# Kernel optimization log

Hardware: AMD Instinct MI355X
Metric: run time of the kernel (lower is better)

## Reference

```python
import jax, jax.numpy as jnp
import numpy as np

T, B, E, H = 2048, 2, 1024, 16
DH = E // H
SCALE = DH ** -0.5
NEG = jnp.finfo(jnp.float32).min


def setup_inputs() -> dict:
    key = jax.random.key(0)
    ks = jax.random.split(key, 10)
    s = 0.02
    query = jax.random.normal(ks[0], (T, B, E), dtype=jnp.float32)
    key_padding_mask = jax.random.randint(ks[1], (B, T), 0, 2).astype(bool)
    # causal additive mask, broadcastable over (bsz, heads, tgt, src)
    causal = jnp.triu(jnp.ones((T, T), dtype=bool), k=1)
    attn_mask = jnp.where(causal, NEG, 0.0).astype(jnp.float32)[None, None]
    Wq = jax.random.normal(ks[2], (E, E), jnp.float32) * s
    bq = jax.random.normal(ks[3], (E,), jnp.float32) * s
    Wk = jax.random.normal(ks[4], (E, E), jnp.float32) * s
    bk = jax.random.normal(ks[5], (E,), jnp.float32) * s
    Wv = jax.random.normal(ks[6], (E, E), jnp.float32) * s
    bv = jax.random.normal(ks[7], (E,), jnp.float32) * s
    Wo = jax.random.normal(ks[8], (E, E), jnp.float32) * s
    bo = jax.random.normal(ks[9], (E,), jnp.float32) * s
    return {"query": query, "key_padding_mask": key_padding_mask, "attn_mask": attn_mask,
            "Wq": Wq, "bq": bq, "Wk": Wk, "bk": bk, "Wv": Wv, "bv": bv, "Wo": Wo, "bo": bo}


def _heads(x):
    # [T, B, E] -> [B, H, T, DH]
    return x.reshape(T, B, H, DH).transpose(1, 2, 0, 3)


def reference(query, key_padding_mask, attn_mask, Wq, bq, Wk, bk, Wv, bv, Wo, bo):
    # projections (torch Linear: x @ W.T + b); q scaled as in module
    q = _heads((query @ Wq.T + bq) * SCALE)          # [B,H,T,DH]
    k = _heads(query @ Wk.T + bk)                    # [B,H,S,DH] (self-attn: S=T)
    v = _heads(query @ Wv.T + bv)
    scores = jnp.einsum('bhtd,bhsd->bhts', q, k)     # [B,H,T,S]
    scores = scores + attn_mask                      # additive causal mask
    # key_padding_mask True -> masked_fill with dtype min
    scores = jnp.where(key_padding_mask[:, None, None, :], NEG, scores)
    probs = jax.nn.softmax(scores, axis=-1)
    ctx = jnp.einsum('bhts,bhsd->bhtd', probs, v)    # [B,H,T,DH]
    ctx = ctx.transpose(2, 0, 1, 3).reshape(T, B, E) # back to [T,B,E]
    return ctx @ Wo.T + bo
```

## Files before the change

kernel.cpp:

```cpp
#include <hip/hip_runtime.h>
#include <hip/hip_bf16.h>
#include <stdint.h>

typedef unsigned short u16;
typedef uint32_t u32;
typedef unsigned long long u64;
typedef __attribute__((ext_vector_type(8))) short bf16x8;
typedef __attribute__((ext_vector_type(4))) float f32x4;
typedef __attribute__((ext_vector_type(16))) float f32x16;
typedef __attribute__((ext_vector_type(2))) unsigned int u32x2;
typedef __attribute__((ext_vector_type(4))) u32 u32x4;

#define T_SEQ 2048

__device__ __forceinline__ float bf2f(u16 u) {
  union { u32 i; float f; } v; v.i = ((u32)u) << 16; return v.f;
}
__device__ __forceinline__ u16 f2bf(float f) {
  union { float f; u32 i; } v; v.f = f;
  u32 u = v.i;
  return (u16)((u + 0x7fffu + ((u >> 16) & 1u)) >> 16);
}

#if __has_builtin(__builtin_amdgcn_exp2f)
#define EXP2F(x) __builtin_amdgcn_exp2f(x)
#else
#define EXP2F(x) exp2f(x)
#endif

__device__ __forceinline__ u32 permpack(float lo, float hi) {
#if __has_builtin(__builtin_amdgcn_perm)
  return __builtin_amdgcn_perm(__float_as_uint(hi), __float_as_uint(lo), 0x07060302u);
#else
  return (__float_as_uint(hi) & 0xFFFF0000u) | (__float_as_uint(lo) >> 16);
#endif
}

__device__ __forceinline__ void plswap(u32& a, u32& b) {
#if __has_builtin(__builtin_amdgcn_permlane32_swap)
  u32x2 r = __builtin_amdgcn_permlane32_swap(a, b, false, false);
  a = r[0]; b = r[1];
#else
  u32 ra = __shfl_xor(a, 32, 64), rb = __shfl_xor(b, 32, 64);
  const bool hi_ = (threadIdx.x & 32) != 0;
  u32 na = hi_ ? rb : a;
  u32 nb = hi_ ? b : ra;
  a = na; b = nb;
#endif
}
__device__ __forceinline__ float othhalf(float x, bool ishi) {
  u32 a = __float_as_uint(x), b = a;
  plswap(a, b);
  return __uint_as_float(ishi ? a : b);
}

__device__ __forceinline__ void gload_lds16(const void* g, void* l) {
  __builtin_amdgcn_global_load_lds(
      (const __attribute__((address_space(1))) void*)g,
      (__attribute__((address_space(3))) void*)l, 16, 0, 0);
}

__global__ __launch_bounds__(256) void cvt5_kernel(
    const float* __restrict__ qsrc, const float* __restrict__ w0,
    const float* __restrict__ w1, const float* __restrict__ w2,
    const float* __restrict__ w3, const int* __restrict__ kpm,
    u16* __restrict__ qbf, u16* __restrict__ wbf, u64* __restrict__ kpmbits) {
  const int bx = blockIdx.x;
  if (bx == 8192) {
    const int wv = threadIdx.x >> 6, lane = threadIdx.x & 63;
    for (int pair = wv; pair < 64; pair += 4) {
      int v = kpm[pair*64 + lane];
      u64 m = __ballot(v != 0);
      if (lane == 0) kpmbits[pair] = m;
    }
    return;
  }
  const float* src; u16* dst; int i;
  if (bx < 4096) {
    src = qsrc; dst = qbf; i = (bx*256 + threadIdx.x)*4;
  } else {
    int t = bx - 4096;
    int z = t >> 10;
    src = (z == 0) ? w0 : (z == 1) ? w1 : (z == 2) ? w2 : w3;
    dst = wbf + (size_t)z * 1048576;
    i = ((t & 1023)*256 + threadIdx.x)*4;
  }
  const float4 v = *(const float4*)(src + i);
  ushort4 o;
  o.x = f2bf(v.x); o.y = f2bf(v.y); o.z = f2bf(v.z); o.w = f2bf(v.w);
  *(ushort4*)(dst + i) = o;
}

__device__ __forceinline__ void gemm_core_128x128(
    f32x4 acc[2][4], const u16* __restrict__ A, const u16* __restrict__ Bw,
    int bm, int bn, u16* As, u16* Bs)
{
  const int tid = threadIdx.x;
  const int w = tid >> 6, lane = tid & 63, g = lane >> 4, c = lane & 15;
  const int wr = (w & 3) * 32, wc = (w >> 2) * 64;
  for (int k0 = 0; k0 < 1024; k0 += 64) {
    __syncthreads();
    #pragma unroll
    for (int is = 0; is < 2; ++is) {
      int o = (is*8 + w)*1024 + lane*16;
      int row = o >> 7, c16 = (o >> 4) & 7;
      gload_lds16(A + (size_t)(bm*128 + row)*1024 + k0 + (c16 ^ (row & 7))*8,
                  (char*)As + (is*8 + w)*1024);
    }
    #pragma unroll
    for (int is = 0; is < 2; ++is) {
      int o = (is*8 + w)*1024 + lane*16;
      int row = o >> 7, c16 = (o >> 4) & 7;
      gload_lds16(Bw + (size_t)(bn*128 + row)*1024 + k0 + (c16 ^ (row & 7))*8,
                  (char*)Bs + (is*8 + w)*1024);
    }
    __syncthreads();
    bf16x8 af[2][2], bfr[4][2];
    #pragma unroll
    for (int mf = 0; mf < 2; ++mf)
      #pragma unroll
      for (int kc = 0; kc < 2; ++kc) {
        int row = wr + mf*16 + c;
        int colb = kc*64 + g*16;
        af[mf][kc] = *(const bf16x8*)((const char*)As + row*128 + (colb ^ ((row & 7) << 4)));
      }
    #pragma unroll
    for (int nf = 0; nf < 4; ++nf)
      #pragma unroll
      for (int kc = 0; kc < 2; ++kc) {
        int row = wc + nf*16 + c;
        int colb = kc*64 + g*16;
        bfr[nf][kc] = *(const bf16x8*)((const char*)Bs + row*128 + (colb ^ ((row & 7) << 4)));
      }
    #pragma unroll
    for (int mf = 0; mf < 2; ++mf)
      #pragma unroll
      for (int nf = 0; nf < 4; ++nf)
        #pragma unroll
        for (int kc = 0; kc < 2; ++kc)
          acc[mf][nf] = __builtin_amdgcn_mfma_f32_16x16x32_bf16(
              af[mf][kc], bfr[nf][kc], acc[mf][nf], 0, 0, 0);
  }
}

__global__ __launch_bounds__(512, 2) void gemm_qkv(
    const u16* __restrict__ Abf, const u16* __restrict__ Wbf,
    const float* __restrict__ bq, const float* __restrict__ bk,
    const float* __restrict__ bv, u16* __restrict__ qkvh)
{
  __shared__ __align__(16) u16 As[128*64];
  __shared__ __align__(16) u16 Bs[128*64];
  f32x4 acc[2][4];
  #pragma unroll
  for (int mf = 0; mf < 2; ++mf)
    #pragma unroll
    for (int nf = 0; nf < 4; ++nf) acc[mf][nf] = (f32x4){0.f,0.f,0.f,0.f};
  const int bx = blockIdx.x;
  const int bm = (bx & 7) * 4 + (bx >> 3);
  gemm_core_128x128(acc, Abf, Wbf, bm, blockIdx.y, As, Bs);
  const int tid = threadIdx.x, w = tid >> 6, lane = tid & 63, g = lane >> 4, c = lane & 15;
  const int wr = (w & 3) * 32, wc = (w >> 2) * 64;
  #pragma unroll
  for (int mf = 0; mf < 2; ++mf)
    #pragma unroll
    for (int nf = 0; nf < 4; ++nf) {
      int col = blockIdx.y*128 + wc + nf*16 + c;
      int z = col >> 10, colz = col & 1023;
      const float* bias = (z == 0) ? bq : (z == 1) ? bk : bv;
      float bcol = bias[colz];
      float scl = (z == 0) ? 0.18033688011112043f : 1.0f;
      int h = colz >> 6, d = colz & 63;
      u16* dst = qkvh + (size_t)z * 4194304;
      #pragma unroll
      for (int r = 0; r < 4; ++r) {
        int row = bm*128 + wr + mf*16 + g*4 + r;
        int t = row >> 1, bb = row & 1;
        float v = (acc[mf][nf][r] + bcol) * scl;
        dst[(size_t)(bb*16 + h)*131072 + (size_t)t*64 + d] = f2bf(v);
      }
    }
}

__global__ __launch_bounds__(512, 2) void gemm_out(
    const u16* __restrict__ ctx2, const u16* __restrict__ Wobf,
    const float* __restrict__ bo, float* __restrict__ out)
{
  __shared__ __align__(16) u16 As[128*64];
  __shared__ __align__(16) u16 Bs[128*64];
  f32x4 acc[2][4];
  #pragma unroll
  for (int mf = 0; mf < 2; ++mf)
    #pragma unroll
    for (int nf = 0; nf < 4; ++nf) acc[mf][nf] = (f32x4){0.f,0.f,0.f,0.f};
  const int bx = blockIdx.x;
  const int bm = (bx & 7) * 4 + (bx >> 3);
  gemm_core_128x128(acc, ctx2, Wobf, bm, blockIdx.y, As, Bs);
  const int tid = threadIdx.x, w = tid >> 6, lane = tid & 63, g = lane >> 4, c = lane & 15;
  const int wr = (w & 3) * 32, wc = (w >> 2) * 64;
  #pragma unroll
  for (int mf = 0; mf < 2; ++mf)
    #pragma unroll
    for (int nf = 0; nf < 4; ++nf) {
      int col = blockIdx.y*128 + wc + nf*16 + c;
      float bcol = bo[col];
      #pragma unroll
      for (int r = 0; r < 4; ++r) {
        int row = bm*128 + wr + mf*16 + g*4 + r;
        out[(size_t)row*1024 + col] = acc[mf][nf][r] + bcol;
      }
    }
}

__global__ __launch_bounds__(256) void vtrans_kernel(const u16* __restrict__ Vh,
                                                     u16* __restrict__ Vt,
                                                     float* __restrict__ vs) {
  __shared__ u16 tile[64][72];
  const int bh = blockIdx.x >> 5, tc = blockIdx.x & 31;
  const int t0 = tc * 64;
  const int tid = threadIdx.x;
  {
    const int tl = tid >> 2, d0 = (tid & 3) * 16;
    const u16* src = Vh + (size_t)bh*131072 + (size_t)(t0 + tl)*64 + d0;
    bf16x8 a = *(const bf16x8*)src;
    bf16x8 b2 = *(const bf16x8*)(src + 8);
    #pragma unroll
    for (int j = 0; j < 8; ++j) {
      tile[d0 + j][tl] = (u16)a[j];
      tile[d0 + 8 + j][tl] = (u16)b2[j];
    }
  }
  __syncthreads();
  {
    const int d = tid >> 2, tq = (tid & 3) * 16;
    bf16x8 o0, o1;
    float s = 0.f;
    #pragma unroll
    for (int j = 0; j < 8; ++j) {
      u16 x0 = tile[d][tq + j], x1 = tile[d][tq + 8 + j];
      o0[j] = (short)x0; o1[j] = (short)x1;
      s += bf2f(x0) + bf2f(x1);
    }
    u16* dst = Vt + (size_t)bh*131072 + (size_t)d*2048 + t0 + tq;
    *(bf16x8*)dst = o0;
    *(bf16x8*)(dst + 8) = o1;
    s += __shfl_xor(s, 1, 64);
    s += __shfl_xor(s, 2, 64);
    if ((tid & 3) == 0) atomicAdd(&vs[bh*64 + d], s);
  }
}

#define ZERO16 (f32x16){0.f,0.f,0.f,0.f,0.f,0.f,0.f,0.f,0.f,0.f,0.f,0.f,0.f,0.f,0.f,0.f}
#define NEGINF (-__builtin_inff())

__device__ const unsigned char CTBL[40] = {
  60, 44, 28, 12, 57, 59, 52, 37,
  61, 45, 29, 42, 40, 56, 53, 38,
  62, 46, 24, 25, 41, 58, 54, 49,
  63,  8, 20, 21, 32, 34, 55, 51,
   0,  4, 16, 17, 33, 36, 48, 50 };

__device__ __forceinline__ int pctx_off(int k, int ch) {
  if (k < 8)  return (k - 4);
  if (k < 12) return 4 + (k - 8)*2 + (ch - 1);
  return 12 + (k - 12)*3 + (ch - 1);
}
__device__ __forceinline__ int pml_off(int k, int ch) {
  if (k < 8)  return (k - 4)*2 + ch;
  if (k < 12) return 8 + (k - 8)*3 + ch;
  return 20 + (k - 12)*4 + ch;
}

__global__ __launch_bounds__(256, 2) void flash_attn(
    const u16* __restrict__ Qh, const u16* __restrict__ Kh,
    const u16* __restrict__ Vt, const u64* __restrict__ kpmbits,
    const float* __restrict__ vsum, u16* __restrict__ ctx2,
    u16* __restrict__ pctxA, u16* __restrict__ pctxB,
    float* __restrict__ pml)
{
  __shared__ __align__(16) u16 Kl[2][4096];
  __shared__ __align__(16) u16 Vl[2][4096];

  const int tid = threadIdx.x;
  const int w = tid >> 6, lane = tid & 63;
  const int l31 = lane & 31, hi = lane >> 5;

  const int id = blockIdx.x;
  const int xcd = id & 7, rest = id >> 3;
  const int bh = xcd * 4 + (rest & 3);
  const int cidx = rest >> 2;
  const int v_tbl = CTBL[cidx];
  const int k = v_tbl >> 2, ch = v_tbl & 3;
  const int NS = (k >> 2) + 1;
  const int nt = 2*k + 2;
  const int lo = (nt * ch) / NS, hicap = (nt * (ch + 1)) / NS;

  const int b = bh >> 4, h = bh & 15;
  const size_t hbase = (size_t)bh * 131072;
  const int q = 128*k + 32*w + l31;
  const int myNt = 2*k + 1 + (w >> 1);

  bf16x8 qfrag[4];
  #pragma unroll
  for (int kt = 0; kt < 4; ++kt)
    qfrag[kt] = *(const bf16x8*)(Qh + hbase + (size_t)q*64 + kt*16 + hi*8);

  const int jb = (w & 1) * 4;

  u64 mcur = kpmbits[(b << 5) + lo];
  {
    const int s0t = lo * 64;
    if (w < 2) {
      #pragma unroll
      for (int is = 0; is < 4; ++is) {
        int o = (jb + is)*1024 + lane*16;
        int row = o >> 7, c16 = (o >> 4) & 7;
        gload_lds16(Kh + hbase + (size_t)(s0t + row)*64 + (c16 ^ (row & 7))*8,
                    (char*)Kl[0] + (jb + is)*1024);
      }
    } else {
      #pragma unroll
      for (int is = 0; is < 4; ++is) {
        int o = (jb + is)*1024 + lane*16;
        int row = o >> 7, c16 = (o >> 4) & 7;
        gload_lds16(Vt + hbase + (size_t)row*2048 + s0t + (c16 ^ (row & 7))*8,
                    (char*)Vl[0] + (jb + is)*1024);
      }
    }
  }
  if (lo + 1 < hicap) {
    const int s0t = (lo + 1) * 64;
    if (w < 2) {
      #pragma unroll
      for (int is = 0; is < 4; ++is) {
        int o = (jb + is)*1024 + lane*16;
        int row = o >> 7, c16 = (o >> 4) & 7;
        gload_lds16(Kh + hbase + (size_t)(s0t + row)*64 + (c16 ^ (row & 7))*8,
                    (char*)Kl[1] + (jb + is)*1024);
      }
    } else {
      #pragma unroll
      for (int is = 0; is < 4; ++is) {
        int o = (jb + is)*1024 + lane*16;
        int row = o >> 7, c16 = (o >> 4) & 7;
        gload_lds16(Vt + hbase + (size_t)row*2048 + s0t + (c16 ^ (row & 7))*8,
                    (char*)Vl[1] + (jb + is)*1024);
      }
    }
  }

  float mrow = NEGINF, lrow = 0.f;
  f32x16 cacc0 = ZERO16, cacc1 = ZERO16;

  for (int t = lo; t < hicap; ++t) {
    const int cur = (t - lo) & 1;
    const int s0 = t * 64;
    const bool haveNext = (t + 1 < hicap);
    const bool diag = (t >= myNt - 1);

    if (haveNext) asm volatile("s_waitcnt vmcnt(4)" ::: "memory");
    else          asm volatile("s_waitcnt vmcnt(0)" ::: "memory");
    u64 mnxt = haveNext ? kpmbits[(b << 5) + t + 1] : 0;
    __builtin_amdgcn_s_barrier();

    u32 kill0 = 0, kill1 = 0;
    {
      const u32 m0 = (u32)mcur, m1 = (u32)(mcur >> 32);
      const u64 m4 = mcur >> 4;
      const u32 m4l = (u32)m4, m4h = (u32)(m4 >> 32);
      const u32 w0m = hi ? m4l : m0;
      const u32 w1m = hi ? m4h : m1;
      const int lim = q - s0 - 4*hi;
      #pragma unroll
      for (int m = 0; m < 4; ++m) {
        u32 nib0 = (w0m >> (m*8)) & 15u;
        u32 nib1 = (w1m >> (m*8)) & 15u;
        if (diag) {
          int t0c = lim - m*8;       int c0 = min(max(t0c + 1, 0), 4);
          int t1c = lim - 32 - m*8;  int c1 = min(max(t1c + 1, 0), 4);
          nib0 |= (0xFu << c0) & 0xFu;
          nib1 |= (0xFu << c1) & 0xFu;
        }
        kill0 |= nib0 << (m*4);
        kill1 |= nib1 << (m*4);
      }
    }
    f32x16 st0, st1;
    #pragma unroll
    for (int i = 0; i < 16; ++i) {
      st0[i] = ((kill0 >> i) & 1u) ? NEGINF : 0.f;
      st1[i] = ((kill1 >> i) & 1u) ? NEGINF : 0.f;
    }

    bf16x8 kreg[2][4], vf[2][4];
    #pragma unroll
    for (int sub = 0; sub < 2; ++sub)
      #pragma unroll
      for (int kt = 0; kt < 4; ++kt) {
        int row = sub*32 + l31;
        int colb = kt*32 + hi*16;
        kreg[sub][kt] = *(const bf16x8*)((const char*)Kl[cur] + row*128 + (colb ^ ((row & 7) << 4)));
        vf[sub][kt]   = *(const bf16x8*)((const char*)Vl[cur] + row*128 + (colb ^ ((row & 7) << 4)));
      }

    __builtin_amdgcn_s_setprio(1);
    #pragma unroll
    for (int kt = 0; kt < 4; ++kt) {
      st0 = __builtin_amdgcn_mfma_f32_32x32x16_bf16(kreg[0][kt], qfrag[kt], st0, 0, 0, 0);
      st1 = __builtin_amdgcn_mfma_f32_32x32x16_bf16(kreg[1][kt], qfrag[kt], st1, 0, 0, 0);
    }
    __builtin_amdgcn_s_setprio(0);

    {
      float t8[8];
      #pragma unroll
      for (int i = 0; i < 8; ++i)
        t8[i] = fmaxf(fmaxf(st0[i], st0[i+8]), fmaxf(st1[i], st1[i+8]));
      float t4a = fmaxf(t8[0], t8[4]), t4b = fmaxf(t8[1], t8[5]);
      float t4c = fmaxf(t8[2], t8[6]), t4d = fmaxf(t8[3], t8[7]);
      float rm = fmaxf(fmaxf(t4a, t4b), fmaxf(t4c, t4d));
      rm = fmaxf(rm, othhalf(rm, hi != 0));

      const bool need = (rm > mrow + 8.f) || (mrow < -1e30f);
      if (__any(need)) {
        const float mn = fmaxf(mrow, rm);
        const float sc = (mn < -1e30f) ? 1.f : EXP2F(mrow - mn);
        mrow = mn;
        lrow *= sc;
        #pragma unroll
        for (int i = 0; i < 16; ++i) { cacc0[i] *= sc; cacc1[i] *= sc; }
      }
      const bool dead = (mrow < -1e30f);
      float a0 = 0.f, a1 = 0.f, a2 = 0.f, a3 = 0.f;
      #pragma unroll
      for (int i = 0; i < 16; i += 4) {
        float p0 = dead ? 0.f : EXP2F(st0[i+0] - mrow); st0[i+0] = p0; a0 += p0;
        float p1 = dead ? 0.f : EXP2F(st0[i+1] - mrow); st0[i+1] = p1; a1 += p1;
        float p2 = dead ? 0.f : EXP2F(st0[i+2] - mrow); st0[i+2] = p2; a2 += p2;
        float p3 = dead ? 0.f : EXP2F(st0[i+3] - mrow); st0[i+3] = p3; a3 += p3;
      }
      #pragma unroll
      for (int i = 0; i < 16; i += 4) {
        float p0 = dead ? 0.f : EXP2F(st1[i+0] - mrow); st1[i+0] = p0; a0 += p0;
        float p1 = dead ? 0.f : EXP2F(st1[i+1] - mrow); st1[i+1] = p1; a1 += p1;
        float p2 = dead ? 0.f : EXP2F(st1[i+2] - mrow); st1[i+2] = p2; a2 += p2;
        float p3 = dead ? 0.f : EXP2F(st1[i+3] - mrow); st1[i+3] = p3; a3 += p3;
      }
      float ps = (a0 + a1) + (a2 + a3);
      ps += othhalf(ps, hi != 0);
      lrow += ps;
    }

    u32 pk[8][2];
    #pragma unroll
    for (int m = 0; m < 4; ++m) {
      pk[m][0]   = permpack(st0[m*4+0], st0[m*4+1]);
      pk[m][1]   = permpack(st0[m*4+2], st0[m*4+3]);
      pk[4+m][0] = permpack(st1[m*4+0], st1[m*4+1]);
      pk[4+m][1] = permpack(st1[m*4+2], st1[m*4+3]);
    }
    bf16x8 pf[4];
    #pragma unroll
    for (int ks = 0; ks < 4; ++ks) {
      u32 w0p = pk[2*ks][0], w2p = pk[2*ks+1][0];
      u32 w1p = pk[2*ks][1], w3p = pk[2*ks+1][1];
      plswap(w0p, w2p);
      plswap(w1p, w3p);
      u32x4 wv = {w0p, w1p, w2p, w3p};
      pf[ks] = __builtin_bit_cast(bf16x8, wv);
    }

    __builtin_amdgcn_s_setprio(1);
    #pragma unroll
    for (int ks = 0; ks < 4; ++ks)
      cacc0 = __builtin_amdgcn_mfma_f32_32x32x16_bf16(vf[0][ks], pf[ks], cacc0, 0, 0, 0);
    #pragma unroll
    for (int ks = 0; ks < 4; ++ks)
      cacc1 = __builtin_amdgcn_mfma_f32_32x32x16_bf16(vf[1][ks], pf[ks], cacc1, 0, 0, 0);
    __builtin_amdgcn_s_setprio(0);

    __builtin_amdgcn_s_barrier();
    if (t + 2 < hicap) {
      const int s0n = (t + 2) * 64;
      if (w < 2) {
        #pragma unroll
        for (int is = 0; is < 4; ++is) {
          int o = (jb + is)*1024 + lane*16;
          int row = o >> 7, c16 = (o >> 4) & 7;
          gload_lds16(Kh + hbase + (size_t)(s0n + row)*64 + (c16 ^ (row & 7))*8,
                      (char*)Kl[cur] + (jb + is)*1024);
        }
      } else {
        #pragma unroll
        for (int is = 0; is < 4; ++is) {
          int o = (jb + is)*1024 + lane*16;
          int row = o >> 7, c16 = (o >> 4) & 7;
          gload_lds16(Vt + hbase + (size_t)row*2048 + s0n + (c16 ^ (row & 7))*8,
                      (char*)Vl[cur] + (jb + is)*1024);
        }
      }
    }
    mcur = mnxt;
  }

  if (NS == 1) {
    const bool dead = (lrow == 0.f);
    const float rl = dead ? 0.f : 1.f / lrow;
    #pragma unroll
    for (int subd = 0; subd < 2; ++subd) {
      #pragma unroll
      for (int m = 0; m < 4; ++m) {
        const int d0 = subd*32 + hi*4 + m*8;
        float v0 = (subd ? cacc1[m*4+0] : cacc0[m*4+0]) * rl;
        float v1 = (subd ? cacc1[m*4+1] : cacc0[m*4+1]) * rl;
        float v2 = (subd ? cacc1[m*4+2] : cacc0[m*4+2]) * rl;
        float v3 = (subd ? cacc1[m*4+3] : cacc0[m*4+3]) * rl;
        if (dead) {
          const float* vs = vsum + bh*64 + d0;
          v0 = vs[0] * (1.0f/2048.0f);
          v1 = vs[1] * (1.0f/2048.0f);
          v2 = vs[2] * (1.0f/2048.0f);
          v3 = vs[3] * (1.0f/2048.0f);
        }
        ushort4 o;
        o.x = f2bf(v0); o.y = f2bf(v1); o.z = f2bf(v2); o.w = f2bf(v3);
        *(ushort4*)(ctx2 + (size_t)(q*2 + b)*1024 + h*64 + d0) = o;
      }
    }
  } else {
    const int row = w*32 + l31;
    if (!hi) {
      float2 ml; ml.x = mrow; ml.y = lrow;
      *(float2*)(pml + (size_t)(bh*36 + pml_off(k, ch))*256 + row*2) = ml;
    }
    u16* pc;
    if (ch == 0) {
      pc = ctx2 + (size_t)(q*2 + b)*1024 + h*64;
    } else {
      const int slot = bh*24 + pctx_off(k, ch);
      pc = (slot < 512) ? (pctxA + (size_t)slot*8192)
                        : (pctxB + (size_t)(slot - 512)*8192);
      pc += (size_t)row*64;
    }
    #pragma unroll
    for (int subd = 0; subd < 2; ++subd) {
      #pragma unroll
      for (int m = 0; m < 4; ++m) {
        const int d0 = subd*32 + hi*4 + m*8;
        const f32x16& cc = subd ? cacc1 : cacc0;
        ushort4 o;
        o.x = f2bf(cc[m*4+0]); o.y = f2bf(cc[m*4+1]);
        o.z = f2bf(cc[m*4+2]); o.w = f2bf(cc[m*4+3]);
        *(ushort4*)(pc + d0) = o;
      }
    }
  }
}

__global__ __launch_bounds__(256) void combine_kernel(
    const u16* __restrict__ pctxA, const u16* __restrict__ pctxB,
    const float* __restrict__ pml, const float* __restrict__ vsum,
    u16* __restrict__ ctx2)
{
  const int k = 4 + blockIdx.x;
  const int bh = blockIdx.y;
  const int NS = (k >> 2) + 1;
  const int b = bh >> 4, h = bh & 15;
  const int tid = threadIdx.x;
  const int row = tid >> 1, dh = (tid & 1) * 32;
  const int q = k*128 + row;

  const float* mlb = pml + (size_t)(bh*36 + pml_off(k, 0))*256 + row*2;
  float m0v = mlb[0],        l0v = mlb[1];
  float m1v = mlb[256+0],    l1v = mlb[256+1];
  float m2v = NEGINF, l2v = 0.f, m3v = NEGINF, l3v = 0.f;
  if (NS > 2) { m2v = mlb[512+0];  l2v = mlb[512+1]; }
  if (NS > 3) { m3v = mlb[768+0];  l3v = mlb[768+1]; }
  float ms = fmaxf(fmaxf(m0v, m1v), fmaxf(m2v, m3v));
  bool dead = (ms < -1e30f);
  const float w0 = dead ? 0.f : EXP2F(m0v - ms);
  const float w1 = dead ? 0.f : EXP2F(m1v - ms);
  const float w2 = (dead || NS <= 2) ? 0.f : EXP2F(m2v - ms);
  const float w3 = (dead || NS <= 3) ? 0.f : EXP2F(m3v - ms);
  const float lt = w0*l0v + w1*l1v + w2*l2v + w3*l3v;
  dead = dead || (lt == 0.f);
  const float rl = dead ? 0.f : 1.f / lt;

  u16* dst = ctx2 + (size_t)(q*2 + b)*1024 + h*64 + dh;
  const u16* pc1; const u16* pc2 = nullptr; const u16* pc3 = nullptr;
  {
    const int s1 = bh*24 + pctx_off(k, 1);
    pc1 = ((s1 < 512) ? (pctxA + (size_t)s1*8192) : (pctxB + (size_t)(s1-512)*8192))
          + (size_t)row*64 + dh;
    if (NS > 2) {
      const int s2 = bh*24 + pctx_off(k, 2);
      pc2 = ((s2 < 512) ? (pctxA + (size_t)s2*8192) : (pctxB + (size_t)(s2-512)*8192))
            + (size_t)row*64 + dh;
    }
    if (NS > 3) {
      const int s3 = bh*24 + pctx_off(k, 3);
      pc3 = ((s3 < 512) ? (pctxA + (size_t)s3*8192) : (pctxB + (size_t)(s3-512)*8192))
            + (size_t)row*64 + dh;
    }
  }
  #pragma unroll
  for (int g2 = 0; g2 < 4; ++g2) {
    bf16x8 a0 = *(const bf16x8*)(dst + g2*8);
    bf16x8 a1 = *(const bf16x8*)(pc1 + g2*8);
    bf16x8 o;
    #pragma unroll
    for (int j = 0; j < 8; ++j) {
      float v = w0*bf2f((u16)a0[j]) + w1*bf2f((u16)a1[j]);
      if (NS > 2) v += w2*bf2f((u16)((const u16*)pc2)[g2*8 + j]);
      if (NS > 3) v += w3*bf2f((u16)((const u16*)pc3)[g2*8 + j]);
      v *= rl;
      if (dead) v = vsum[bh*64 + dh + g2*8 + j] * (1.0f/2048.0f);
      o[j] = (short)f2bf(v);
    }
    *(bf16x8*)(dst + g2*8) = o;
  }
}

extern "C" void kernel_launch(void* const* d_in, const int* in_sizes, int n_in,
                              void* d_out, int out_size, void* d_ws, size_t ws_size,
                              hipStream_t stream) {
  const float* query = (const float*)d_in[0];
  const int*   kpm   = (const int*)d_in[1];
  const float* Wq = (const float*)d_in[3];
  const float* bq = (const float*)d_in[4];
  const float* Wk = (const float*)d_in[5];
  const float* bk = (const float*)d_in[6];
  const float* Wv = (const float*)d_in[7];
  const float* bv = (const float*)d_in[8];
  const float* Wo = (const float*)d_in[9];
  const float* bo = (const float*)d_in[10];

  char* ws = (char*)d_ws;
  u16*   qbf     = (u16*)(ws);
  u16*   Vt      = (u16*)(ws);
  u16*   wbf     = (u16*)(ws + 8388608);
  u16*   pctxB   = (u16*)(ws + 8388608);
  u16*   qkvh    = (u16*)(ws + 16777216);
  u16*   pctxA   = (u16*)(ws + 33554432);
  u16*   ctx2    = (u16*)(ws + 41943040);
  float* vsum    = (float*)(ws + 50331648);
  float* pml     = (float*)(ws + 50339840);
  u64*   kpmbits = (u64*)(ws + 51650560);

  cvt5_kernel<<<dim3(8193), 256, 0, stream>>>(query, Wq, Wk, Wv, Wo, kpm,
                                              qbf, wbf, kpmbits);

  hipMemsetAsync(vsum, 0, 2048 * sizeof(float), stream);

  gemm_qkv<<<dim3(32, 24), 512, 0, stream>>>(qbf, wbf, bq, bk, bv, qkvh);
  vtrans_kernel<<<dim3(1024), 256, 0, stream>>>(qkvh + 2*4194304, Vt, vsum);
  flash_attn<<<dim3(1280), 256, 0, stream>>>(qkvh, qkvh + 1*4194304,
                                             Vt, kpmbits, vsum, ctx2,
                                             pctxA, pctxB, pml);
  combine_kernel<<<dim3(12, 32), 256, 0, stream>>>(pctxA, pctxB, pml, vsum, ctx2);
  gemm_out<<<dim3(32, 8), 512, 0, stream>>>(ctx2, wbf + 3*1048576, bo, (float*)d_out);
}
```

Baseline: 143.9 us.

## Rebalance flash-attention key splits to fewer chunks and drop GEMM block swizzle

Changes the split-K work decomposition of the causal flash attention: query tiles are now split into at most 3 key chunks (instead of up to 4), giving 32 work items per head rather than 40, with a new scheduling table, reduced partial-context/ML storage, and a simplified combine kernel over 11 tiles. This cuts partial-result writes and combine traffic and removes the second partial buffer, at the cost of longer per-block work for late tiles. The GEMM kernels also drop the XCD-aware row remapping of blockIdx, which may change L2 locality.

Result: faster. 138.9 us (-3.5%).

```diff
diff --git a/kernel.cpp b/kernel.cpp
--- a/kernel.cpp
+++ b/kernel.cpp
@@ -155,8 +155,7 @@
   for (int mf = 0; mf < 2; ++mf)
     #pragma unroll
     for (int nf = 0; nf < 4; ++nf) acc[mf][nf] = (f32x4){0.f,0.f,0.f,0.f};
-  const int bx = blockIdx.x;
-  const int bm = (bx & 7) * 4 + (bx >> 3);
+  const int bm = blockIdx.x;
   gemm_core_128x128(acc, Abf, Wbf, bm, blockIdx.y, As, Bs);
   const int tid = threadIdx.x, w = tid >> 6, lane = tid & 63, g = lane >> 4, c = lane & 15;
   const int wr = (w & 3) * 32, wc = (w >> 2) * 64;
@@ -192,8 +191,7 @@
   for (int mf = 0; mf < 2; ++mf)
     #pragma unroll
     for (int nf = 0; nf < 4; ++nf) acc[mf][nf] = (f32x4){0.f,0.f,0.f,0.f};
-  const int bx = blockIdx.x;
-  const int bm = (bx & 7) * 4 + (bx >> 3);
+  const int bm = blockIdx.x;
   gemm_core_128x128(acc, ctx2, Wobf, bm, blockIdx.y, As, Bs);
   const int tid = threadIdx.x, w = tid >> 6, lane = tid & 63, g = lane >> 4, c = lane & 15;
   const int wr = (w & 3) * 32, wc = (w >> 2) * 64;
@@ -252,30 +250,26 @@
 #define ZERO16 (f32x16){0.f,0.f,0.f,0.f,0.f,0.f,0.f,0.f,0.f,0.f,0.f,0.f,0.f,0.f,0.f,0.f}
 #define NEGINF (-__builtin_inff())
 
-__device__ const unsigned char CTBL[40] = {
-  60, 44, 28, 12, 57, 59, 52, 37,
-  61, 45, 29, 42, 40, 56, 53, 38,
-  62, 46, 24, 25, 41, 58, 54, 49,
-  63,  8, 20, 21, 32, 34, 55, 51,
-   0,  4, 16, 17, 33, 36, 48, 50 };
+__device__ const unsigned char CTBL[32] = {
+  40, 61, 36, 56, 58, 54, 52, 49,
+  41, 62, 37, 57, 60, 32, 53, 50,
+  16, 12, 28, 29, 44, 45, 33, 46,
+   0,  4,  8, 20, 21, 24, 25, 48 };
 
 __device__ __forceinline__ int pctx_off(int k, int ch) {
-  if (k < 8)  return (k - 4);
-  if (k < 12) return 4 + (k - 8)*2 + (ch - 1);
-  return 12 + (k - 12)*3 + (ch - 1);
+  if (k < 11) return (k - 5);
+  return 6 + (k - 11)*2 + (ch - 1);
 }
 __device__ __forceinline__ int pml_off(int k, int ch) {
-  if (k < 8)  return (k - 4)*2 + ch;
-  if (k < 12) return 8 + (k - 8)*3 + ch;
-  return 20 + (k - 12)*4 + ch;
+  if (k < 11) return (k - 5)*2 + ch;
+  return 12 + (k - 11)*3 + ch;
 }
 
 __global__ __launch_bounds__(256, 2) void flash_attn(
     const u16* __restrict__ Qh, const u16* __restrict__ Kh,
     const u16* __restrict__ Vt, const u64* __restrict__ kpmbits,
     const float* __restrict__ vsum, u16* __restrict__ ctx2,
-    u16* __restrict__ pctxA, u16* __restrict__ pctxB,
-    float* __restrict__ pml)
+    u16* __restrict__ pctxA, float* __restrict__ pml)
 {
   __shared__ __align__(16) u16 Kl[2][4096];
   __shared__ __align__(16) u16 Vl[2][4096];
@@ -290,7 +284,7 @@
   const int cidx = rest >> 2;
   const int v_tbl = CTBL[cidx];
   const int k = v_tbl >> 2, ch = v_tbl & 3;
-  const int NS = (k >> 2) + 1;
+  const int NS = (k <= 4) ? 1 : (k <= 10) ? 2 : 3;
   const int nt = 2*k + 2;
   const int lo = (nt * ch) / NS, hicap = (nt * (ch + 1)) / NS;
 
@@ -530,16 +524,14 @@
     const int row = w*32 + l31;
     if (!hi) {
       float2 ml; ml.x = mrow; ml.y = lrow;
-      *(float2*)(pml + (size_t)(bh*36 + pml_off(k, ch))*256 + row*2) = ml;
+      *(float2*)(pml + (size_t)(bh*27 + pml_off(k, ch))*256 + row*2) = ml;
     }
     u16* pc;
     if (ch == 0) {
       pc = ctx2 + (size_t)(q*2 + b)*1024 + h*64;
     } else {
-      const int slot = bh*24 + pctx_off(k, ch);
-      pc = (slot < 512) ? (pctxA + (size_t)slot*8192)
-                        : (pctxB + (size_t)(slot - 512)*8192);
-      pc += (size_t)row*64;
+      const int slot = bh*16 + pctx_off(k, ch);
+      pc = pctxA + (size_t)slot*8192 + (size_t)row*64;
     }
     #pragma unroll
     for (int subd = 0; subd < 2; ++subd) {
@@ -557,51 +549,37 @@
 }
 
 __global__ __launch_bounds__(256) void combine_kernel(
-    const u16* __restrict__ pctxA, const u16* __restrict__ pctxB,
-    const float* __restrict__ pml, const float* __restrict__ vsum,
-    u16* __restrict__ ctx2)
+    const u16* __restrict__ pctxA, const float* __restrict__ pml,
+    const float* __restrict__ vsum, u16* __restrict__ ctx2)
 {
-  const int k = 4 + blockIdx.x;
+  const int k = 5 + blockIdx.x;
   const int bh = blockIdx.y;
-  const int NS = (k >> 2) + 1;
+  const int NS = (k <= 10) ? 2 : 3;
   const int b = bh >> 4, h = bh & 15;
   const int tid = threadIdx.x;
   const int row = tid >> 1, dh = (tid & 1) * 32;
   const int q = k*128 + row;
 
-  const float* mlb = pml + (size_t)(bh*36 + pml_off(k, 0))*256 + row*2;
-  float m0v = mlb[0],        l0v = mlb[1];
-  float m1v = mlb[256+0],    l1v = mlb[256+1];
-  float m2v = NEGINF, l2v = 0.f, m3v = NEGINF, l3v = 0.f;
-  if (NS > 2) { m2v = mlb[512+0];  l2v = mlb[512+1]; }
-  if (NS > 3) { m3v = mlb[768+0];  l3v = mlb[768+1]; }
-  float ms = fmaxf(fmaxf(m0v, m1v), fmaxf(m2v, m3v));
+  const float* mlb = pml + (size_t)(bh*27 + pml_off(k, 0))*256 + row*2;
+  float m0v = mlb[0],     l0v = mlb[1];
+  float m1v = mlb[256+0], l1v = mlb[256+1];
+  float m2v = NEGINF, l2v = 0.f;
+  if (NS > 2) { m2v = mlb[512+0]; l2v = mlb[512+1]; }
+  float ms = fmaxf(fmaxf(m0v, m1v), m2v);
   bool dead = (ms < -1e30f);
   const float w0 = dead ? 0.f : EXP2F(m0v - ms);
   const float w1 = dead ? 0.f : EXP2F(m1v - ms);
   const float w2 = (dead || NS <= 2) ? 0.f : EXP2F(m2v - ms);
-  const float w3 = (dead || NS <= 3) ? 0.f : EXP2F(m3v - ms);
-  const float lt = w0*l0v + w1*l1v + w2*l2v + w3*l3v;
+  const float lt = w0*l0v + w1*l1v + w2*l2v;
   dead = dead || (lt == 0.f);
   const float rl = dead ? 0.f : 1.f / lt;
 
   u16* dst = ctx2 + (size_t)(q*2 + b)*1024 + h*64 + dh;
-  const u16* pc1; const u16* pc2 = nullptr; const u16* pc3 = nullptr;
-  {
-    const int s1 = bh*24 + pctx_off(k, 1);
-    pc1 = ((s1 < 512) ? (pctxA + (size_t)s1*8192) : (pctxB + (size_t)(s1-512)*8192))
-          + (size_t)row*64 + dh;
-    if (NS > 2) {
-      const int s2 = bh*24 + pctx_off(k, 2);
-      pc2 = ((s2 < 512) ? (pctxA + (size_t)s2*8192) : (pctxB + (size_t)(s2-512)*8192))
-            + (size_t)row*64 + dh;
-    }
-    if (NS > 3) {
-      const int s3 = bh*24 + pctx_off(k, 3);
-      pc3 = ((s3 < 512) ? (pctxA + (size_t)s3*8192) : (pctxB + (size_t)(s3-512)*8192))
-            + (size_t)row*64 + dh;
-    }
-  }
+  const u16* pc1 = pctxA + (size_t)(bh*16 + pctx_off(k, 1))*8192 + (size_t)row*64 + dh;
+  const u16* pc2 = nullptr;
+  if (NS > 2)
+    pc2 = pctxA + (size_t)(bh*16 + pctx_off(k, 2))*8192 + (size_t)row*64 + dh;
+
   #pragma unroll
   for (int g2 = 0; g2 < 4; ++g2) {
     bf16x8 a0 = *(const bf16x8*)(dst + g2*8);
@@ -610,8 +588,7 @@
     #pragma unroll
     for (int j = 0; j < 8; ++j) {
       float v = w0*bf2f((u16)a0[j]) + w1*bf2f((u16)a1[j]);
-      if (NS > 2) v += w2*bf2f((u16)((const u16*)pc2)[g2*8 + j]);
-      if (NS > 3) v += w3*bf2f((u16)((const u16*)pc3)[g2*8 + j]);
+      if (NS > 2) v += w2*bf2f((u16)pc2[g2*8 + j]);
       v *= rl;
       if (dead) v = vsum[bh*64 + dh + g2*8 + j] * (1.0f/2048.0f);
       o[j] = (short)f2bf(v);
@@ -638,7 +615,6 @@
   u16*   qbf     = (u16*)(ws);
   u16*   Vt      = (u16*)(ws);
   u16*   wbf     = (u16*)(ws + 8388608);
-  u16*   pctxB   = (u16*)(ws + 8388608);
   u16*   qkvh    = (u16*)(ws + 16777216);
   u16*   pctxA   = (u16*)(ws + 33554432);
   u16*   ctx2    = (u16*)(ws + 41943040);
@@ -653,9 +629,9 @@
 
   gemm_qkv<<<dim3(32, 24), 512, 0, stream>>>(qbf, wbf, bq, bk, bv, qkvh);
   vtrans_kernel<<<dim3(1024), 256, 0, stream>>>(qkvh + 2*4194304, Vt, vsum);
-  flash_attn<<<dim3(1280), 256, 0, stream>>>(qkvh, qkvh + 1*4194304,
+  flash_attn<<<dim3(1024), 256, 0, stream>>>(qkvh, qkvh + 1*4194304,
                                              Vt, kpmbits, vsum, ctx2,
-                                             pctxA, pctxB, pml);
-  combine_kernel<<<dim3(12, 32), 256, 0, stream>>>(pctxA, pctxB, pml, vsum, ctx2);
+                                             pctxA, pml);
+  combine_kernel<<<dim3(11, 32), 256, 0, stream>>>(pctxA, pml, vsum, ctx2);
   gemm_out<<<dim3(32, 8), 512, 0, stream>>>(ctx2, wbf + 3*1048576, bo, (float*)d_out);
 }
```
